# Kernel optimization log

Hardware: AMD Instinct MI355X
Metric: run time of the kernel (lower is better)

The kernel has to match this reference:

```python
import jax, jax.numpy as jnp
import numpy as np

B, S, D, H = 2, 2048, 1024, 16
HD = D // H
EPS = 1e-5


def setup_inputs() -> dict:
    key = jax.random.key(0)
    ks = jax.random.split(key, 12)
    s = 1.0 / np.sqrt(D)
    inp = {
        "q": jax.random.normal(ks[0], (B, S, D), jnp.float32),
        "k": jax.random.normal(ks[1], (B, S, D), jnp.float32),
        "v": jax.random.normal(ks[2], (B, S, D), jnp.float32),
        "mask": jnp.ones((B, S, S), jnp.int32),
        "Wq": jax.random.normal(ks[3], (D, D), jnp.float32) * s,
        "bq": jnp.zeros((D,), jnp.float32),
        "Wk": jax.random.normal(ks[4], (D, D), jnp.float32) * s,
        "bk": jnp.zeros((D,), jnp.float32),
        "Wv": jax.random.normal(ks[5], (D, D), jnp.float32) * s,
        "bv": jnp.zeros((D,), jnp.float32),
        "Wo": jax.random.normal(ks[6], (D, D), jnp.float32) * s,
        "bo": jnp.zeros((D,), jnp.float32),
        "gamma": jnp.ones((D,), jnp.float32),
        "beta": jnp.zeros((D,), jnp.float32),
    }
    return inp


def reference(q, k, v, mask, Wq, bq, Wk, bk, Wv, bv, Wo, bo, gamma, beta):
    residual = q
    # projections (torch Linear: x @ W.T + b)
    qh = (q @ Wq.T + bq).reshape(B, S, H, HD).transpose(0, 2, 1, 3)  # b h s d
    kh = (k @ Wk.T + bk).reshape(B, S, H, HD).transpose(0, 2, 1, 3)
    vh = (v @ Wv.T + bv).reshape(B, S, H, HD).transpose(0, 2, 1, 3)
    scores = jnp.einsum('bhid,bhjd->bhij', qh, kh) / jnp.sqrt(jnp.float32(HD))
    scores = jnp.where(mask[:, None, :, :] == 0, jnp.float32(-1e9), scores)
    attention = jax.nn.softmax(scores, axis=-1)  # dropout=0 (eval)
    context = jnp.einsum('bhij,bhjd->bhid', attention, vh)
    context = context.transpose(0, 2, 1, 3).reshape(B, S, D)
    out = context @ Wo.T + bo
    x = out + residual
    mu = jnp.mean(x, axis=-1, keepdims=True)
    var = jnp.mean(jnp.square(x - mu), axis=-1, keepdims=True)
    output = (x - mu) * jax.lax.rsqrt(var + EPS) * gamma + beta
    return (output, attention)
```

## Files before the change

kernel.cpp:

```cpp
#include <hip/hip_runtime.h>
#include <hip/hip_bf16.h>


typedef float f32x4 __attribute__((ext_vector_type(4)));
typedef short short8 __attribute__((ext_vector_type(8)));

#if __has_builtin(__builtin_amdgcn_exp2f)
#define EXP2(x) __builtin_amdgcn_exp2f(x)
#else
#define EXP2(x) exp2f(x)
#endif

#define QSCALE 0.18033688011112042f
#define MASKNEG -1.4426950408889634e9f

__device__ __forceinline__ short f2bs(float f) {
  union { __hip_bfloat16 h; short s; } u;
  u.h = __float2bfloat16(f);
  return u.s;
}

__device__ __forceinline__ void async16(const void* g, void* l) {
  __builtin_amdgcn_global_load_lds(
      (const __attribute__((address_space(1))) unsigned int*)g,
      (__attribute__((address_space(3))) unsigned int*)l, 16, 0, 0);
}

__global__ __launch_bounds__(256) void cvt_kernel(
    const float* __restrict__ q, const float* __restrict__ k, const float* __restrict__ v,
    const float* __restrict__ wq, const float* __restrict__ wk, const float* __restrict__ wv,
    const float* __restrict__ wo, short* __restrict__ dst) {
  long base = (long)blockIdx.x * 2048;
  const float* src;
  if      (base <  4194304) src = q  + base;
  else if (base <  8388608) src = k  + (base - 4194304);
  else if (base < 12582912) src = v  + (base - 8388608);
  else if (base < 13631488) src = wq + (base - 12582912);
  else if (base < 14680064) src = wk + (base - 13631488);
  else if (base < 15728640) src = wv + (base - 14680064);
  else                      src = wo + (base - 15728640);
  int off = threadIdx.x * 8;
  float4 a = *(const float4*)(src + off);
  float4 b = *(const float4*)(src + off + 4);
  short8 o;
  o[0] = f2bs(a.x); o[1] = f2bs(a.y); o[2] = f2bs(a.z); o[3] = f2bs(a.w);
  o[4] = f2bs(b.x); o[5] = f2bs(b.y); o[6] = f2bs(b.z); o[7] = f2bs(b.w);
  *(short8*)(dst + base + off) = o;
}

__global__ __launch_bounds__(256) void mask_kernel(const int* __restrict__ mask,
                                                   unsigned* __restrict__ bits,
                                                   unsigned* __restrict__ flags) {
  int t = threadIdx.x, w = t >> 6, lane = t & 63;
  for (int it = 0; it < 16; ++it) {
    long gw = (long)it * 8192 + blockIdx.x * 4 + w;
    long base = gw * 64;
    int v = mask[base + lane];
    unsigned long long m = __ballot(v != 0);
    if (lane == 0)  bits[gw * 2]     = (unsigned)m;
    if (lane == 32) bits[gw * 2 + 1] = (unsigned)(m >> 32);
    if (lane == 0 && m != 0xFFFFFFFFFFFFFFFFull) {
      long j = base & 2047, i = (base >> 11) & 2047, b = base >> 22;
      atomicOr(&flags[(int)(b * 256 + (i >> 7) * 16 + (j >> 7))], 1u);
    }
  }
}

__global__ __launch_bounds__(256, 2) void proj_kernel(
    const short* __restrict__ Abase, const short* __restrict__ Wbase,
    const float* __restrict__ bq, const float* __restrict__ bk, const float* __restrict__ bv,
    short* __restrict__ Qh, short* __restrict__ Kh, short* __restrict__ Vt) {
  __shared__ __align__(16) short As[128 * 64];
  __shared__ __align__(16) short Bs[128 * 64];
  const int mode = blockIdx.z;
  const short* A = Abase + (size_t)mode * 4194304;
  const short* W = Wbase + (size_t)mode * 1048576;
  const float* bias = (mode == 0) ? bq : (mode == 1 ? bk : bv);
  const int t = threadIdx.x, w = t >> 6, lane = t & 63, g = lane >> 4, lc = lane & 15;
  const int wrow = (w >> 1) * 64, wcol = (w & 1) * 64;
  const int m0 = blockIdx.x * 128, n0 = blockIdx.y * 128;
  f32x4 acc[4][4] = {};
  for (int kt = 0; kt < 16; ++kt) {
    const int k0 = kt * 64;
    __syncthreads();
#pragma unroll
    for (int i = 0; i < 4; i++) {
      int cb = i * 256 + w * 64, ch = cb + lane, row = ch >> 3, c = ch & 7;
      async16(A + (size_t)(m0 + row) * 1024 + k0 + ((c ^ (row & 7)) << 3), (void*)&As[cb << 3]);
    }
#pragma unroll
    for (int i = 0; i < 4; i++) {
      int cb = i * 256 + w * 64, ch = cb + lane, row = ch >> 3, c = ch & 7;
      async16(W + (size_t)(n0 + row) * 1024 + k0 + ((c ^ (row & 7)) << 3), (void*)&Bs[cb << 3]);
    }
    __syncthreads();
#pragma unroll
    for (int kf = 0; kf < 2; ++kf) {
      short8 af[4], bf[4];
#pragma unroll
      for (int m = 0; m < 4; m++) {
        int row = wrow + m * 16 + lc;
        af[m] = *(const short8*)&As[(row << 6) + (((kf * 4 + g) ^ (row & 7)) << 3)];
      }
#pragma unroll
      for (int n = 0; n < 4; n++) {
        int row = wcol + n * 16 + lc;
        bf[n] = *(const short8*)&Bs[(row << 6) + (((kf * 4 + g) ^ (row & 7)) << 3)];
      }
#pragma unroll
      for (int m = 0; m < 4; m++)
#pragma unroll
        for (int n = 0; n < 4; n++)
          acc[m][n] = __builtin_amdgcn_mfma_f32_16x16x32_bf16(af[m], bf[n], acc[m][n], 0, 0, 0);
    }
  }
#pragma unroll
  for (int n = 0; n < 4; n++) {
    const int col = n0 + wcol + n * 16 + lc;
    const float bv_ = bias[col];
    const int h = col >> 6, d = col & 63;
#pragma unroll
    for (int m = 0; m < 4; m++)
#pragma unroll
      for (int r = 0; r < 4; r++) {
        const int srow = m0 + wrow + m * 16 + g * 4 + r;
        const int b = srow >> 11, s = srow & 2047;
        float val = acc[m][n][r] + bv_;
        if (mode == 0)
          Qh[((size_t)(b * 16 + h) * 2048 + s) * 64 + d] = f2bs(val * QSCALE);
        else if (mode == 1)
          Kh[((size_t)(b * 16 + h) * 2048 + s) * 64 + d] = f2bs(val);
        else
          Vt[((size_t)(b * 16 + h) * 64 + d) * 2048 + s] = f2bs(val);
      }
  }
}

__global__ __launch_bounds__(256, 2) void attn_kernel(
    const short* __restrict__ Qh, const short* __restrict__ Kh, const short* __restrict__ Vt,
    const unsigned* __restrict__ mbits, const unsigned* __restrict__ mflags,
    float* __restrict__ Pout, short* __restrict__ ctx) {
  __shared__ __align__(16) short Ks[2][128 * 64];
  __shared__ __align__(16) short Vs[64 * 128];
  __shared__ __align__(16) short Ps[128 * 128];
  const int L = blockIdx.x;
  const int xcd = L & 7, idx = L >> 3;
  const int bh = xcd + ((idx >> 4) << 3);
  const int qb = idx & 15;
  const int b = bh >> 4, h = bh & 15;
  const int t = threadIdx.x, w = t >> 6, lane = t & 63, g = lane >> 4, lc = lane & 15;
  const short* Qp = Qh + (size_t)bh * 2048 * 64;
  const short* Kp = Kh + (size_t)bh * 2048 * 64;
  const short* Vp = Vt + (size_t)bh * 64 * 2048;
  float* Pb = Pout + ((size_t)bh * 2048 + qb * 128) * 2048;

  short8 qf[2][2];
#pragma unroll
  for (int qm = 0; qm < 2; qm++)
#pragma unroll
    for (int kf = 0; kf < 2; kf++)
      qf[qm][kf] = *(const short8*)(Qp + (size_t)(qb * 128 + w * 32 + qm * 16 + lc) * 64 + kf * 32 + g * 8);

#define STAGE_K(buf, j0)                                                                   \
  do {                                                                                     \
    _Pragma("unroll") for (int i_ = 0; i_ < 4; i_++) {                                     \
      int cb = i_ * 256 + w * 64, ch = cb + lane, row = ch >> 3, c = ch & 7;               \
      int sc = c ^ (row & 7) ^ ((row >> 3) & 7);                                           \
      async16(Kp + (size_t)((j0) + row) * 64 + (sc << 3), (void*)&Ks[buf][cb << 3]);       \
    }                                                                                      \
  } while (0)
#define STAGE_V(j0)                                                                        \
  do {                                                                                     \
    _Pragma("unroll") for (int i_ = 0; i_ < 4; i_++) {                                     \
      int cb = i_ * 256 + w * 64, ch = cb + lane, row = ch >> 4, c = ch & 15;              \
      async16(Vp + (size_t)row * 2048 + (j0) + ((c ^ (row & 15)) << 3), (void*)&Vs[cb << 3]); \
    }                                                                                      \
  } while (0)

  float lsum[2] = {0.f, 0.f};
  int kb = 0;
  STAGE_K(0, 0);
  __syncthreads();
  for (int it = 0; it < 16; ++it) {
    if (it < 15) STAGE_K(kb ^ 1, (it + 1) * 128);
    f32x4 acc[2][8] = {};
#pragma unroll
    for (int kf = 0; kf < 2; kf++)
#pragma unroll
      for (int n = 0; n < 8; n++) {
        int row = n * 16 + lc;
        int sc = (kf * 4 + g) ^ (row & 7) ^ ((row >> 3) & 7);
        short8 kfr = *(const short8*)&Ks[kb][(row << 6) + (sc << 3)];
        acc[0][n] = __builtin_amdgcn_mfma_f32_16x16x32_bf16(kfr, qf[0][kf], acc[0][n], 0, 0, 0);
        acc[1][n] = __builtin_amdgcn_mfma_f32_16x16x32_bf16(kfr, qf[1][kf], acc[1][n], 0, 0, 0);
      }
    unsigned flg = mflags[b * 256 + qb * 16 + it];
    if (flg) {
#pragma unroll
      for (int qm = 0; qm < 2; qm++) {
        int ig = qb * 128 + w * 32 + qm * 16 + lc;
        uint4 mw = *(const uint4*)(mbits + ((size_t)b * 2048 + ig) * 64 + it * 4);
#pragma unroll
        for (int n = 0; n < 8; n++) {
          unsigned bw = (n >> 1) == 0 ? mw.x : ((n >> 1) == 1 ? mw.y : ((n >> 1) == 2 ? mw.z : mw.w));
#pragma unroll
          for (int r = 0; r < 4; r++)
            if (!((bw >> (((n & 1) << 4) + g * 4 + r)) & 1u)) acc[qm][n][r] = MASKNEG;
        }
      }
    }
#pragma unroll
    for (int qm = 0; qm < 2; qm++) {
      float s_ = 0.f;
#pragma unroll
      for (int n = 0; n < 8; n++)
#pragma unroll
        for (int r = 0; r < 4; r++) s_ += EXP2(acc[qm][n][r]);
      s_ += __shfl_xor(s_, 16);
      s_ += __shfl_xor(s_, 32);
      lsum[qm] += s_;
    }
    __syncthreads();
    kb ^= 1;
  }
  float* ls = (float*)Vs;
  if (g == 0) { ls[w * 32 + lc] = lsum[0]; ls[w * 32 + 16 + lc] = lsum[1]; }
  __syncthreads();
  float linv[8];
#pragma unroll
  for (int qm = 0; qm < 2; qm++)
#pragma unroll
    for (int r = 0; r < 4; r++) linv[qm * 4 + r] = 1.0f / ls[w * 32 + qm * 16 + g * 4 + r];
  kb = 0;
  STAGE_K(0, 0);
  __syncthreads();

  f32x4 acco[2][4] = {};
  for (int it = 0; it < 16; ++it) {
    const int j0 = it * 128;
    STAGE_V(j0);
    if (it < 15) STAGE_K(kb ^ 1, j0 + 128);
    f32x4 accs[2][8] = {};
#pragma unroll
    for (int kf = 0; kf < 2; kf++)
#pragma unroll
      for (int n = 0; n < 8; n++) {
        int row = lc * 8 + n;
        int sc = (kf * 4 + g) ^ n ^ (lc & 7);
        short8 kfr = *(const short8*)&Ks[kb][(row << 6) + (sc << 3)];
        accs[0][n] = __builtin_amdgcn_mfma_f32_16x16x32_bf16(qf[0][kf], kfr, accs[0][n], 0, 0, 0);
        accs[1][n] = __builtin_amdgcn_mfma_f32_16x16x32_bf16(qf[1][kf], kfr, accs[1][n], 0, 0, 0);
      }
    unsigned flg = mflags[b * 256 + qb * 16 + it];
    if (flg) {
#pragma unroll
      for (int qm = 0; qm < 2; qm++)
#pragma unroll
        for (int r = 0; r < 4; r++) {
          int ig = qb * 128 + w * 32 + qm * 16 + g * 4 + r;
          uint4 mw = *(const uint4*)(mbits + ((size_t)b * 2048 + ig) * 64 + it * 4);
          unsigned w01 = (lc & 4) ? mw.y : mw.x;
          unsigned w23 = (lc & 4) ? mw.w : mw.z;
          unsigned wsel = (lc & 8) ? w23 : w01;
#pragma unroll
          for (int n = 0; n < 8; n++)
            if (!((wsel >> (((lc & 3) << 3) + n)) & 1u)) accs[qm][n][r] = MASKNEG;
        }
    }
#pragma unroll
    for (int qm = 0; qm < 2; qm++)
#pragma unroll
      for (int r = 0; r < 4; r++) {
        const float li = linv[qm * 4 + r];
        const int irow = w * 32 + qm * 16 + g * 4 + r;
        f32x4 p0, p1;
#pragma unroll
        for (int n = 0; n < 4; n++) p0[n] = EXP2(accs[qm][n][r]) * li;
#pragma unroll
        for (int n = 0; n < 4; n++) p1[n] = EXP2(accs[qm][n + 4][r]) * li;
        float* pr = Pb + (size_t)irow * 2048 + j0 + (lc << 3);
        *(f32x4*)pr = p0;
        *(f32x4*)(pr + 4) = p1;
        short8 pk;
#pragma unroll
        for (int n = 0; n < 4; n++) { pk[n] = f2bs(p0[n]); pk[n + 4] = f2bs(p1[n]); }
        *(short8*)&Ps[(irow << 7) + ((lc ^ (irow & 15)) << 3)] = pk;
      }
    __syncthreads();
#pragma unroll
    for (int kt4 = 0; kt4 < 4; kt4++) {
      short8 pa[2];
#pragma unroll
      for (int qm = 0; qm < 2; qm++) {
        int row = w * 32 + qm * 16 + lc;
        pa[qm] = *(const short8*)&Ps[(row << 7) + ((((kt4 << 2) + g) ^ (row & 15)) << 3)];
      }
#pragma unroll
      for (int dn = 0; dn < 4; dn++) {
        int d = dn * 16 + lc;
        short8 vb_ = *(const short8*)&Vs[(d << 7) + ((((kt4 << 2) + g) ^ (d & 15)) << 3)];
        acco[0][dn] = __builtin_amdgcn_mfma_f32_16x16x32_bf16(pa[0], vb_, acco[0][dn], 0, 0, 0);
        acco[1][dn] = __builtin_amdgcn_mfma_f32_16x16x32_bf16(pa[1], vb_, acco[1][dn], 0, 0, 0);
      }
    }
    __syncthreads();
    kb ^= 1;
  }
#pragma unroll
  for (int qm = 0; qm < 2; qm++)
#pragma unroll
    for (int dn = 0; dn < 4; dn++)
#pragma unroll
      for (int r = 0; r < 4; r++) {
        int srow = qb * 128 + w * 32 + qm * 16 + g * 4 + r;
        int col = h * 64 + dn * 16 + lc;
        ctx[(size_t)(b * 2048 + srow) * 1024 + col] = f2bs(acco[qm][dn][r]);
      }
#undef STAGE_K
#undef STAGE_V
}

__global__ __launch_bounds__(256, 2) void oproj_kernel(
    const short* __restrict__ A, const short* __restrict__ W,
    const float* __restrict__ bo, const float* __restrict__ qres, float* __restrict__ xo) {
  __shared__ __align__(16) short As[128 * 64];
  __shared__ __align__(16) short Bs[128 * 64];
  const int t = threadIdx.x, w = t >> 6, lane = t & 63, g = lane >> 4, lc = lane & 15;
  const int wrow = (w >> 1) * 64, wcol = (w & 1) * 64;
  const int m0 = blockIdx.x * 128, n0 = blockIdx.y * 128;
  f32x4 acc[4][4] = {};
  for (int kt = 0; kt < 16; ++kt) {
    const int k0 = kt * 64;
    __syncthreads();
#pragma unroll
    for (int i = 0; i < 4; i++) {
      int cb = i * 256 + w * 64, ch = cb + lane, row = ch >> 3, c = ch & 7;
      async16(A + (size_t)(m0 + row) * 1024 + k0 + ((c ^ (row & 7)) << 3), (void*)&As[cb << 3]);
    }
#pragma unroll
    for (int i = 0; i < 4; i++) {
      int cb = i * 256 + w * 64, ch = cb + lane, row = ch >> 3, c = ch & 7;
      async16(W + (size_t)(n0 + row) * 1024 + k0 + ((c ^ (row & 7)) << 3), (void*)&Bs[cb << 3]);
    }
    __syncthreads();
#pragma unroll
    for (int kf = 0; kf < 2; ++kf) {
      short8 af[4], bf[4];
#pragma unroll
      for (int m = 0; m < 4; m++) {
        int row = wrow + m * 16 + lc;
        af[m] = *(const short8*)&As[(row << 6) + (((kf * 4 + g) ^ (row & 7)) << 3)];
      }
#pragma unroll
      for (int n = 0; n < 4; n++) {
        int row = wcol + n * 16 + lc;
        bf[n] = *(const short8*)&Bs[(row << 6) + (((kf * 4 + g) ^ (row & 7)) << 3)];
      }
#pragma unroll
      for (int m = 0; m < 4; m++)
#pragma unroll
        for (int n = 0; n < 4; n++)
          acc[m][n] = __builtin_amdgcn_mfma_f32_16x16x32_bf16(af[m], bf[n], acc[m][n], 0, 0, 0);
    }
  }
#pragma unroll
  for (int n = 0; n < 4; n++) {
    const int col = n0 + wcol + n * 16 + lc;
    const float bv_ = bo[col];
#pragma unroll
    for (int m = 0; m < 4; m++)
#pragma unroll
      for (int r = 0; r < 4; r++) {
        const int srow = m0 + wrow + m * 16 + g * 4 + r;
        size_t o = (size_t)srow * 1024 + col;
        xo[o] = acc[m][n][r] + bv_ + qres[o];
      }
  }
}

__global__ __launch_bounds__(256) void ln_kernel(const float* __restrict__ x,
                                                 const float* __restrict__ gamma,
                                                 const float* __restrict__ beta,
                                                 float* __restrict__ out) {
  const int row = blockIdx.x, t = threadIdx.x;
  const float4 v = ((const float4*)(x + (size_t)row * 1024))[t];
  float s = v.x + v.y + v.z + v.w;
  float sq = v.x * v.x + v.y * v.y + v.z * v.z + v.w * v.w;
#pragma unroll
  for (int off = 1; off < 64; off <<= 1) { s += __shfl_xor(s, off); sq += __shfl_xor(sq, off); }
  __shared__ float ss[4], sqs[4];
  const int w = t >> 6, lane = t & 63;
  if (lane == 0) { ss[w] = s; sqs[w] = sq; }
  __syncthreads();
  s = ss[0] + ss[1] + ss[2] + ss[3];
  sq = sqs[0] + sqs[1] + sqs[2] + sqs[3];
  const float mu = s * (1.f / 1024.f);
  const float var = sq * (1.f / 1024.f) - mu * mu;
  const float rs = rsqrtf(var + 1e-5f);
  const float4 gm = ((const float4*)gamma)[t];
  const float4 bt = ((const float4*)beta)[t];
  float4 o;
  o.x = (v.x - mu) * rs * gm.x + bt.x;
  o.y = (v.y - mu) * rs * gm.y + bt.y;
  o.z = (v.z - mu) * rs * gm.z + bt.z;
  o.w = (v.w - mu) * rs * gm.w + bt.w;
  ((float4*)(out + (size_t)row * 1024))[t] = o;
}

extern "C" void kernel_launch(void* const* d_in, const int* in_sizes, int n_in,
                              void* d_out, int out_size, void* d_ws, size_t ws_size,
                              hipStream_t stream) {
  (void)in_sizes; (void)n_in; (void)out_size; (void)ws_size;
  const float* q     = (const float*)d_in[0];
  const float* k     = (const float*)d_in[1];
  const float* v     = (const float*)d_in[2];
  const int*   mask  = (const int*)d_in[3];
  const float* Wq    = (const float*)d_in[4];
  const float* bq    = (const float*)d_in[5];
  const float* Wk    = (const float*)d_in[6];
  const float* bk    = (const float*)d_in[7];
  const float* Wv    = (const float*)d_in[8];
  const float* bv    = (const float*)d_in[9];
  const float* Wo    = (const float*)d_in[10];
  const float* bo    = (const float*)d_in[11];
  const float* gamma = (const float*)d_in[12];
  const float* beta  = (const float*)d_in[13];

  char* ws = (char*)d_ws;
  short* cvtdst = (short*)ws;
  short* Qh     = (short*)(ws + 33554432);
  short* Kh     = (short*)(ws + 41943040);
  short* Vt     = (short*)(ws + 50331648);
  unsigned* mbits  = (unsigned*)(ws + 58720256);
  unsigned* mflags = (unsigned*)(ws + 59768832);
  float* x   = (float*)ws;
  short* ctx = (short*)(ws + 16777216);

  float* outln = (float*)d_out;
  float* Pout  = (float*)d_out + 4194304;

  hipMemsetAsync(mflags, 0, 2048, stream);
  cvt_kernel<<<8192, 256, 0, stream>>>(q, k, v, Wq, Wk, Wv, Wo, cvtdst);
  mask_kernel<<<2048, 256, 0, stream>>>(mask, mbits, mflags);
  proj_kernel<<<dim3(32, 8, 3), 256, 0, stream>>>(cvtdst, cvtdst + 12582912, bq, bk, bv, Qh, Kh, Vt);
  attn_kernel<<<512, 256, 0, stream>>>(Qh, Kh, Vt, mbits, mflags, Pout, ctx);
  oproj_kernel<<<dim3(32, 8), 256, 0, stream>>>(ctx, cvtdst + 15728640, bo, q, x);
  ln_kernel<<<4096, 256, 0, stream>>>(x, gamma, beta, outln);
}
```

Before: 283.3 us.

## Merge cvt and mask kernels, relax attention barriers, add MFMA priority and nontemporal stores

```diff
diff --git a/kernel.cpp b/kernel.cpp
--- a/kernel.cpp
+++ b/kernel.cpp
@@ -14,6 +14,9 @@
 #define QSCALE 0.18033688011112042f
 #define MASKNEG -1.4426950408889634e9f
 
+#define BAR_DRAIN16() asm volatile("s_waitcnt vmcnt(16) lgkmcnt(0)\ns_barrier" ::: "memory")
+#define BAR_LGKM()    asm volatile("s_waitcnt lgkmcnt(0)\ns_barrier" ::: "memory")
+
 __device__ __forceinline__ short f2bs(float f) {
   union { __hip_bfloat16 h; short s; } u;
   u.h = __float2bfloat16(f);
@@ -26,42 +29,42 @@
       (__attribute__((address_space(3))) unsigned int*)l, 16, 0, 0);
 }
 
-__global__ __launch_bounds__(256) void cvt_kernel(
+__global__ __launch_bounds__(256) void cvt_mask_kernel(
     const float* __restrict__ q, const float* __restrict__ k, const float* __restrict__ v,
     const float* __restrict__ wq, const float* __restrict__ wk, const float* __restrict__ wv,
-    const float* __restrict__ wo, short* __restrict__ dst) {
-  long base = (long)blockIdx.x * 2048;
-  const float* src;
-  if      (base <  4194304) src = q  + base;
-  else if (base <  8388608) src = k  + (base - 4194304);
-  else if (base < 12582912) src = v  + (base - 8388608);
-  else if (base < 13631488) src = wq + (base - 12582912);
-  else if (base < 14680064) src = wk + (base - 13631488);
-  else if (base < 15728640) src = wv + (base - 14680064);
-  else                      src = wo + (base - 15728640);
-  int off = threadIdx.x * 8;
-  float4 a = *(const float4*)(src + off);
-  float4 b = *(const float4*)(src + off + 4);
-  short8 o;
-  o[0] = f2bs(a.x); o[1] = f2bs(a.y); o[2] = f2bs(a.z); o[3] = f2bs(a.w);
-  o[4] = f2bs(b.x); o[5] = f2bs(b.y); o[6] = f2bs(b.z); o[7] = f2bs(b.w);
-  *(short8*)(dst + base + off) = o;
-}
-
-__global__ __launch_bounds__(256) void mask_kernel(const int* __restrict__ mask,
-                                                   unsigned* __restrict__ bits,
-                                                   unsigned* __restrict__ flags) {
-  int t = threadIdx.x, w = t >> 6, lane = t & 63;
-  for (int it = 0; it < 16; ++it) {
-    long gw = (long)it * 8192 + blockIdx.x * 4 + w;
-    long base = gw * 64;
-    int v = mask[base + lane];
-    unsigned long long m = __ballot(v != 0);
-    if (lane == 0)  bits[gw * 2]     = (unsigned)m;
-    if (lane == 32) bits[gw * 2 + 1] = (unsigned)(m >> 32);
-    if (lane == 0 && m != 0xFFFFFFFFFFFFFFFFull) {
-      long j = base & 2047, i = (base >> 11) & 2047, b = base >> 22;
-      atomicOr(&flags[(int)(b * 256 + (i >> 7) * 16 + (j >> 7))], 1u);
+    const float* __restrict__ wo, short* __restrict__ dst,
+    const int* __restrict__ mask, unsigned* __restrict__ bits, unsigned* __restrict__ flags) {
+  if (blockIdx.x < 8192) {
+    long base = (long)blockIdx.x * 2048;
+    const float* src;
+    if      (base <  4194304) src = q  + base;
+    else if (base <  8388608) src = k  + (base - 4194304);
+    else if (base < 12582912) src = v  + (base - 8388608);
+    else if (base < 13631488) src = wq + (base - 12582912);
+    else if (base < 14680064) src = wk + (base - 13631488);
+    else if (base < 15728640) src = wv + (base - 14680064);
+    else                      src = wo + (base - 15728640);
+    int off = threadIdx.x * 8;
+    float4 a = *(const float4*)(src + off);
+    float4 b = *(const float4*)(src + off + 4);
+    short8 o;
+    o[0] = f2bs(a.x); o[1] = f2bs(a.y); o[2] = f2bs(a.z); o[3] = f2bs(a.w);
+    o[4] = f2bs(b.x); o[5] = f2bs(b.y); o[6] = f2bs(b.z); o[7] = f2bs(b.w);
+    *(short8*)(dst + base + off) = o;
+  } else {
+    int bid = blockIdx.x - 8192;
+    int t = threadIdx.x, w = t >> 6, lane = t & 63;
+    for (int it = 0; it < 16; ++it) {
+      long gw = (long)it * 8192 + bid * 4 + w;
+      long base = gw * 64;
+      int mv = mask[base + lane];
+      unsigned long long m = __ballot(mv != 0);
+      if (lane == 0)  bits[gw * 2]     = (unsigned)m;
+      if (lane == 32) bits[gw * 2 + 1] = (unsigned)(m >> 32);
+      if (lane == 0 && m != 0xFFFFFFFFFFFFFFFFull) {
+        long j = base & 2047, i = (base >> 11) & 2047, b = base >> 22;
+        atomicOr(&flags[(int)(b * 256 + (i >> 7) * 16 + (j >> 7))], 1u);
+      }
     }
   }
 }
@@ -184,6 +187,7 @@
   for (int it = 0; it < 16; ++it) {
     if (it < 15) STAGE_K(kb ^ 1, (it + 1) * 128);
     f32x4 acc[2][8] = {};
+    __builtin_amdgcn_s_setprio(1);
 #pragma unroll
     for (int kf = 0; kf < 2; kf++)
 #pragma unroll
@@ -194,6 +198,7 @@
         acc[0][n] = __builtin_amdgcn_mfma_f32_16x16x32_bf16(kfr, qf[0][kf], acc[0][n], 0, 0, 0);
         acc[1][n] = __builtin_amdgcn_mfma_f32_16x16x32_bf16(kfr, qf[1][kf], acc[1][n], 0, 0, 0);
       }
+    __builtin_amdgcn_s_setprio(0);
     unsigned flg = mflags[b * 256 + qb * 16 + it];
     if (flg) {
 #pragma unroll
@@ -241,6 +246,7 @@
     STAGE_V(j0);
     if (it < 15) STAGE_K(kb ^ 1, j0 + 128);
     f32x4 accs[2][8] = {};
+    __builtin_amdgcn_s_setprio(1);
 #pragma unroll
     for (int kf = 0; kf < 2; kf++)
 #pragma unroll
@@ -251,6 +257,7 @@
         accs[0][n] = __builtin_amdgcn_mfma_f32_16x16x32_bf16(qf[0][kf], kfr, accs[0][n], 0, 0, 0);
         accs[1][n] = __builtin_amdgcn_mfma_f32_16x16x32_bf16(qf[1][kf], kfr, accs[1][n], 0, 0, 0);
       }
+    __builtin_amdgcn_s_setprio(0);
     unsigned flg = mflags[b * 256 + qb * 16 + it];
     if (flg) {
 #pragma unroll
@@ -278,15 +285,16 @@
         for (int n = 0; n < 4; n++) p0[n] = EXP2(accs[qm][n][r]) * li;
 #pragma unroll
         for (int n = 0; n < 4; n++) p1[n] = EXP2(accs[qm][n + 4][r]) * li;
-        float* pr = Pb + (size_t)irow * 2048 + j0 + (lc << 3);
-        *(f32x4*)pr = p0;
-        *(f32x4*)(pr + 4) = p1;
+        f32x4* pr = (f32x4*)(Pb + (size_t)irow * 2048 + j0 + (lc << 3));
+        __builtin_nontemporal_store(p0, pr);
+        __builtin_nontemporal_store(p1, pr + 1);
         short8 pk;
 #pragma unroll
         for (int n = 0; n < 4; n++) { pk[n] = f2bs(p0[n]); pk[n + 4] = f2bs(p1[n]); }
         *(short8*)&Ps[(irow << 7) + ((lc ^ (irow & 15)) << 3)] = pk;
       }
-    __syncthreads();
+    BAR_DRAIN16();
+    __builtin_amdgcn_s_setprio(1);
 #pragma unroll
     for (int kt4 = 0; kt4 < 4; kt4++) {
       short8 pa[2];
@@ -303,7 +311,8 @@
         acco[1][dn] = __builtin_amdgcn_mfma_f32_16x16x32_bf16(pa[1], vb_, acco[1][dn], 0, 0, 0);
       }
     }
-    __syncthreads();
+    __builtin_amdgcn_s_setprio(0);
+    BAR_LGKM();
     kb ^= 1;
   }
 #pragma unroll
@@ -440,8 +449,7 @@
   float* Pout  = (float*)d_out + 4194304;
 
   hipMemsetAsync(mflags, 0, 2048, stream);
-  cvt_kernel<<<8192, 256, 0, stream>>>(q, k, v, Wq, Wk, Wv, Wo, cvtdst);
-  mask_kernel<<<2048, 256, 0, stream>>>(mask, mbits, mflags);
+  cvt_mask_kernel<<<10240, 256, 0, stream>>>(q, k, v, Wq, Wk, Wv, Wo, cvtdst, mask, mbits, mflags);
   proj_kernel<<<dim3(32, 8, 3), 256, 0, stream>>>(cvtdst, cvtdst + 12582912, bq, bk, bv, Qh, Kh, Vt);
   attn_kernel<<<512, 256, 0, stream>>>(Qh, Kh, Vt, mbits, mflags, Pout, ctx);
   oproj_kernel<<<dim3(32, 8), 256, 0, stream>>>(ctx, cvtdst + 15728640, bo, q, x);
```

New measurement: 379.3 us. 33.9% more time.
